# Performance work log

Hardware: AMD Instinct MI355X
Metric: run time of the kernel (lower is better)

Reference implementation:

```python
import jax, jax.numpy as jnp
import numpy as np

B, N, XD = 64, 512, 32  # batch, n_points, x_dims (feature columns); last 2 cols are t, y


def setup_inputs() -> dict:
    key = jax.random.key(0)
    xtys = jax.random.normal(key, (B, N, XD + 2), dtype=jnp.float32)
    return {"xtys": xtys}


def _linear_dml(xtys):
    b, n, D = xtys.shape
    d = D - 2
    xs = xtys[..., :d]          # (b, n, d) covariates
    ts = xtys[..., d]           # (b, n)   treatment
    ys = xtys[..., d + 1]       # (b, n)   outcome

    # Growing-prefix least squares via cumulative sufficient statistics.
    # For prefix i (rows 0..i): min-norm lstsq solution w = pinv(X^T X) X^T v == pinv(X) v,
    # matching torch.linalg.lstsq (gelsy/gelsd) semantics including rank-deficient prefixes.
    G = jnp.cumsum(jnp.einsum('bnd,bne->bnde', xs, xs), axis=1)      # (b,n,d,d) Gram
    Xty = jnp.cumsum(xs * ys[..., None], axis=1)                     # (b,n,d)
    Xtt = jnp.cumsum(xs * ts[..., None], axis=1)                     # (b,n,d)
    Sty = jnp.cumsum(ts * ys, axis=1)                                # (b,n)
    Stt = jnp.cumsum(ts * ts, axis=1)                                # (b,n)

    Ginv = jnp.linalg.pinv(G)                                        # batched pinv, (b,n,d,d)
    wy = jnp.einsum('bnde,bne->bnd', Ginv, Xty)
    wt = jnp.einsum('bnde,bne->bnd', Ginv, Xtt)

    # ate_i = <t_res, y_res> / <t_res, t_res> over prefix, expanded via the stats above.
    num = (Sty
           - jnp.einsum('bnd,bnd->bn', wt, Xty)
           - jnp.einsum('bnd,bnd->bn', wy, Xtt)
           + jnp.einsum('bnd,bnde,bne->bn', wt, G, wy))
    den = (Stt
           - 2.0 * jnp.einsum('bnd,bnd->bn', wt, Xtt)
           + jnp.einsum('bnd,bnde,bne->bn', wt, G, wt))
    safe = den > 0
    ate = jnp.where(safe, num / jnp.where(safe, den, 1.0), 0.0)      # min-norm: 0 when thats==0

    means = ate.at[:, 0].set(0.0)                                    # i==0 special case
    stds = jnp.zeros_like(means)                                     # module always appends zeros
    return means, 2.0 * jnp.log(stds)                                # -> -inf, as in the original


def reference(xtys):
    return _linear_dml(xtys)
```

## Files before the change

### kernel.cpp

```cpp
#include <hip/hip_runtime.h>
#include <math.h>
#include <utility>

#define BB 64
#define NN 512
#define DD 32
#define ZD 34
#define NE 595
#define WIN 8
#define NW 64
#define WACT 60

#define SEG 4
#define RS 128
#define KWS 16
#define CH 4
#define ECH 149
#define PSTRIDE 17

#define SPW 4

__device__ inline void ent2ij(int e, int& i, int& j) {
    int ii = 0, rem = e;
    while (rem >= ZD - ii) { rem -= (ZD - ii); ++ii; }
    i = ii; j = ii + rem;
}

template<int N> struct Pack { Pack<N - 1> head; float v; };
template<> struct Pack<1> { float v; };
template<int I, int N> __device__ __forceinline__ float& pget(Pack<N>& p) {
    static_assert(I < N, "oob");
    if constexpr (I == N - 1) return p.v;
    else return pget<I, N - 1>(p.head);
}

__device__ __forceinline__ float rdlane(float x, int srclane) {
    return __int_as_float(__builtin_amdgcn_readlane(__float_as_int(x), srclane));
}

__global__ __launch_bounds__(256) void dml_gram(const float* __restrict__ xtys,
                                                float* __restrict__ P,
                                                float* __restrict__ out) {
    const int t   = threadIdx.x;
    const int blk = blockIdx.x;
    const int c   = blk % CH;
    const int bg  = blk / CH;
    const int g   = bg % SEG;
    const int b   = bg / SEG;

    const int gid = blk * 256 + t;
    if (gid < BB * NN) out[BB * NN + gid] = 0.0f;
    if (gid < BB * DD) out[(gid >> 5) * NN + (gid & 31)] = 0.0f;

    __shared__ float zs[RS * ZD];
    const float* src = xtys + ((size_t)b * NN + (size_t)g * RS) * ZD;
    for (int u = t; u < RS * ZD; u += 256) zs[u] = src[u];
    __syncthreads();

    const int e = c * ECH + t;
    if (t < ECH && e < NE) {
        int i, j;
        ent2ij(e, i, j);
        float* pdst = P + (size_t)(b * SEG + g) * PSTRIDE * NE + e;
        double acc = 0.0;
#pragma unroll
        for (int k = 0; k < KWS; ++k) {
            pdst[k * NE] = (float)acc;
#pragma unroll
            for (int s8 = 0; s8 < WIN; ++s8) {
                const float* row = &zs[(k * WIN + s8) * ZD];
                acc = fma((double)row[i], (double)row[j], acc);
            }
        }
        pdst[KWS * NE] = (float)acc;
    }
}


template<int R> __device__ __forceinline__
float initval(int j, const float* snL, const float* zb) {
    if constexpr (R < DD) {
        float v = 0.0f;
        if (j < DD) {
            int i0 = (R < j) ? R : j;
            int j0 = (R < j) ? j : R;
            v = snL[i0 * ZD - (i0 * (i0 - 1)) / 2 + (j0 - i0)];
        } else if (j < DD + WIN) {
            v = zb[(j - DD) * ZD + R];
        } else if (j == 40) {
            v = snL[R * ZD - (R * (R - 1)) / 2 + (DD - R)];
        } else if (j == 41) {
            v = snL[R * ZD - (R * (R - 1)) / 2 + (DD + 1 - R)];
        }
        return v;
    } else if constexpr (R < DD + WIN) {
        return (j < DD) ? zb[(R - DD) * ZD + j] : 0.0f;
    } else if constexpr (R == 40) {
        return (j < DD) ? snL[j * ZD - (j * (j - 1)) / 2 + (DD - j)] : 0.0f;
    } else if constexpr (R == 41) {
        return (j < DD) ? snL[j * ZD - (j * (j - 1)) / 2 + (DD + 1 - j)] : 0.0f;
    } else {
        return 0.0f;
    }
}
template<int R> __device__ __forceinline__
void init_rec(Pack<48>& A, int j, const float* snL, const float* zb) {
    if constexpr (R < 48) {
        pget<R>(A) = initval<R>(j, snL, zb);
        init_rec<R + 1>(A, j, snL, zb);
    }
}

template<int K, int R> __device__ __forceinline__
void elim_rows(Pack<48>& A, float t) {
    if constexpr (R < DD + 10) {
        float fr = rdlane(pget<R>(A), K);
        pget<R>(A) = fmaf(-fr, t, pget<R>(A));
        elim_rows<K, R + 1>(A, t);
    }
}
template<int K> __device__ __forceinline__
void elim_step(Pack<48>& A) {
    float piv  = rdlane(pget<K>(A), K);
    float invp = (piv > 1e-30f) ? 1.0f / piv : 0.0f;
    float t    = invp * pget<K>(A);
    elim_rows<K, K + 1>(A, t);
}
template<int... Ks> __device__ __forceinline__
void elim_all(Pack<48>& A, std::integer_sequence<int, Ks...>) {
    ((elim_step<Ks>(A)), ...);
}

template<int R> __device__ __forceinline__
void kdump(Pack<48>& A, float* Kl, int c) {
    if constexpr (R < DD + 10) {
        Kl[(R - DD) * 10 + c] = -pget<R>(A);
        kdump<R + 1>(A, Kl, c);
    }
}

template<int L> __device__ __forceinline__
void tinit(Pack<96>& T, int m, const float* Kl, const float* zb) {
    if constexpr (L < 96) {
        constexpr int I = L / 12, J = L % 12;
        float v;
        if constexpr (J < 8) {
            float kij = (I < m && J < m) ? Kl[I * 10 + J] : 0.0f;
            v = kij + ((I == J) ? 1.0f : 0.0f);
        } else if constexpr (J == 8)  v = (I < m) ? Kl[I * 10 + 8] : 0.0f;
        else if constexpr (J == 9)    v = (I < m) ? zb[I * ZD + DD] : 0.0f;
        else if constexpr (J == 10)   v = (I < m) ? Kl[I * 10 + 9] : 0.0f;
        else                          v = (I < m) ? zb[I * ZD + DD + 1] : 0.0f;
        pget<L>(T) = v;
        tinit<L + 1>(T, m, Kl, zb);
    }
}
template<int K, int I, int J> __device__ __forceinline__
void gj_cols(Pack<96>& T, float f) {
    if constexpr (J < 12) {
        pget<I * 12 + J>(T) = fmaf(-f, pget<K * 12 + J>(T), pget<I * 12 + J>(T));
        gj_cols<K, I, J + 1>(T, f);
    }
}
template<int K, int I> __device__ __forceinline__
void gj_rows(Pack<96>& T, float invp) {
    if constexpr (I < 8) {
        if constexpr (I != K) {
            float f = pget<I * 12 + K>(T) * invp;
            gj_cols<K, I, K + 1>(T, f);
        }
        gj_rows<K, I + 1>(T, invp);
    }
}
template<int K> __device__ __forceinline__
void gj_step(Pack<96>& T) {
    float piv  = pget<K * 12 + K>(T);
    float invp = (piv > 1e-30f || piv < -1e-30f) ? 1.0f / piv : 0.0f;
    gj_rows<K, 0>(T, invp);
}
template<int... Ks> __device__ __forceinline__
void gj_all(Pack<96>& T, std::integer_sequence<int, Ks...>) {
    ((gj_step<Ks>(T)), ...);
}
template<int I> __device__ __forceinline__
void finacc(Pack<96>& T, int m, const float* Kl, const float* zb,
            double& dt, double& nt) {
    if constexpr (I < 8) {
        if (I < m) {
            float di   = pget<I * 12 + I>(T);
            float dinv = (di > 1e-30f || di < -1e-30f) ? 1.0f / di : 0.0f;
            double s1 = (double)(pget<I * 12 + 8>(T) * dinv);
            double s2 = (double)(pget<I * 12 + 9>(T) * dinv);
            double r1 = (double)(pget<I * 12 + 10>(T) * dinv);
            double r2 = (double)(pget<I * 12 + 11>(T) * dinv);
            double g  = (double)Kl[80 + I] - (double)zb[I * ZD + DD];
            dt += g * (s1 - s2);
            nt += g * (r1 - r2);
        }
        finacc<I + 1>(T, m, Kl, zb, dt, nt);
    }
}

__global__ __launch_bounds__(256) void dml_solve(const float* __restrict__ xtys,
                                                 const float* __restrict__ P,
                                                 float* __restrict__ out) {
    const int wid  = threadIdx.x >> 6;
    const int lane = threadIdx.x & 63;
    const int id   = blockIdx.x * SPW + wid;
    const int w    = (id % WACT) + 4;
    const int b    = id / WACT;
    const int g    = w >> 4;
    const int k    = w & 15;

    __shared__ float snL[SPW][NE];
    __shared__ float zb[SPW][WIN * ZD];
    __shared__ float Kl[SPW][100];
    float* snW = snL[wid];
    float* zbW = zb[wid];
    float* KlW = Kl[wid];

    const float* pb  = P + (size_t)b * SEG * PSTRIDE * NE;
    const float* src = xtys + ((size_t)b * NN + (size_t)w * WIN) * ZD;
    for (int u = lane; u < NE; u += 64) {
        float v = pb[(size_t)(g * PSTRIDE + k) * NE + u];
        for (int g2 = 0; g2 < g; ++g2)
            v += pb[(size_t)(g2 * PSTRIDE + KWS) * NE + u];
        snW[u] = v;
    }
    for (int u = lane; u < WIN * ZD; u += 64) zbW[u] = src[u];
    __syncthreads();

    Pack<48> A;
    init_rec<0>(A, lane, snW, zbW);

    elim_all(A, std::make_integer_sequence<int, DD>{});

    if (lane >= DD && lane < DD + 10) kdump<DD>(A, KlW, lane - DD);
    __syncthreads();

    if (lane < 8) {
        const int m = lane + 1;
        Pack<96> T;
        tinit<0>(T, m, KlW, zbW);
        gj_all(T, std::make_integer_sequence<int, 8>{});
        double dt = 0.0, nt = 0.0;
        finacc<0>(T, m, KlW, zbW, dt, nt);
        double Stt0 = (double)snW[592];
        double Sty0 = (double)snW[593];
        double den  = Stt0 - (double)KlW[88] + dt;
        double num  = Sty0 - (double)KlW[89] + nt;
        double val  = (den > 0.0) ? num / den : 0.0;
        if (!isfinite(val)) val = 0.0;
        out[b * NN + w * WIN + lane] = (float)val;
    }
}

extern "C" void kernel_launch(void* const* d_in, const int* in_sizes, int n_in,
                              void* d_out, int out_size, void* d_ws, size_t ws_size,
                              hipStream_t stream) {
    const float* xtys = (const float*)d_in[0];
    float* out = (float*)d_out;
    float* P = (float*)d_ws;

    hipLaunchKernelGGL(dml_gram, dim3(BB * SEG * CH), dim3(256), 0, stream, xtys, P, out);
    hipLaunchKernelGGL(dml_solve, dim3(BB * WACT / SPW), dim3(256), 0, stream, xtys, P, out);
}
```

Baseline: 108.7 us.

## Spread the small Gauss-Jordan solves across all wave lanes with bpermute

The final 8x12 Gauss-Jordan solve previously ran on only 8 lanes, each keeping a 96-float tableau in registers. It is now split so each of the 64 lanes owns one row of one of the 8 systems. Pivot rows are fetched with ds_bpermute and the per-system sums are reduced with width-8 xor shuffles. The change also precomputes the triangular-index offsets used when loading the Gram matrix. It drops the two block barriers and relies on each wave using only its own shared-memory slice, which cuts register pressure and serial tail work but depends on intra-wave LDS ordering for correctness.

After: 98.08 us. 1.11x faster.

```diff
diff --git a/kernel.cpp b/kernel.cpp
--- a/kernel.cpp
+++ b/kernel.cpp
@@ -36,6 +36,9 @@
 
 __device__ __forceinline__ float rdlane(float x, int srclane) {
     return __int_as_float(__builtin_amdgcn_readlane(__float_as_int(x), srclane));
+}
+__device__ __forceinline__ float bperm(int byteaddr, float x) {
+    return __int_as_float(__builtin_amdgcn_ds_bpermute(byteaddr, __float_as_int(x)));
 }
 
 __global__ __launch_bounds__(256) void dml_gram(const float* __restrict__ xtys,
@@ -78,36 +81,37 @@
 
 
 template<int R> __device__ __forceinline__
-float initval(int j, const float* snL, const float* zb) {
+float initval(int j, int off_j, int zoff, const float* snL, const float* zb) {
+    constexpr int RC = (R < DD) ? (R * ZD - (R * (R - 1)) / 2 - R) : 0;
     if constexpr (R < DD) {
         float v = 0.0f;
         if (j < DD) {
-            int i0 = (R < j) ? R : j;
-            int j0 = (R < j) ? j : R;
-            v = snL[i0 * ZD - (i0 * (i0 - 1)) / 2 + (j0 - i0)];
+            int idx = (R < j) ? (RC + j) : (off_j + R);
+            v = snL[idx];
         } else if (j < DD + WIN) {
-            v = zb[(j - DD) * ZD + R];
+            v = zb[zoff + R];
         } else if (j == 40) {
-            v = snL[R * ZD - (R * (R - 1)) / 2 + (DD - R)];
+            v = snL[RC + DD];
         } else if (j == 41) {
-            v = snL[R * ZD - (R * (R - 1)) / 2 + (DD + 1 - R)];
+            v = snL[RC + DD + 1];
         }
         return v;
     } else if constexpr (R < DD + WIN) {
         return (j < DD) ? zb[(R - DD) * ZD + j] : 0.0f;
     } else if constexpr (R == 40) {
-        return (j < DD) ? snL[j * ZD - (j * (j - 1)) / 2 + (DD - j)] : 0.0f;
+        return (j < DD) ? snL[off_j + DD] : 0.0f;
     } else if constexpr (R == 41) {
-        return (j < DD) ? snL[j * ZD - (j * (j - 1)) / 2 + (DD + 1 - j)] : 0.0f;
+        return (j < DD) ? snL[off_j + DD + 1] : 0.0f;
     } else {
         return 0.0f;
     }
 }
 template<int R> __device__ __forceinline__
-void init_rec(Pack<48>& A, int j, const float* snL, const float* zb) {
+void init_rec(Pack<48>& A, int j, int off_j, int zoff,
+              const float* snL, const float* zb) {
     if constexpr (R < 48) {
-        pget<R>(A) = initval<R>(j, snL, zb);
-        init_rec<R + 1>(A, j, snL, zb);
+        pget<R>(A) = initval<R>(j, off_j, zoff, snL, zb);
+        init_rec<R + 1>(A, j, off_j, zoff, snL, zb);
     }
 }
 
@@ -140,65 +144,40 @@
 }
 
 template<int L> __device__ __forceinline__
-void tinit(Pack<96>& T, int m, const float* Kl, const float* zb) {
-    if constexpr (L < 96) {
-        constexpr int I = L / 12, J = L % 12;
+void tinit(Pack<12>& T, int row, int sys, const float* Kl, const float* zb) {
+    if constexpr (L < 12) {
         float v;
-        if constexpr (J < 8) {
-            float kij = (I < m && J < m) ? Kl[I * 10 + J] : 0.0f;
-            v = kij + ((I == J) ? 1.0f : 0.0f);
-        } else if constexpr (J == 8)  v = (I < m) ? Kl[I * 10 + 8] : 0.0f;
-        else if constexpr (J == 9)    v = (I < m) ? zb[I * ZD + DD] : 0.0f;
-        else if constexpr (J == 10)   v = (I < m) ? Kl[I * 10 + 9] : 0.0f;
-        else                          v = (I < m) ? zb[I * ZD + DD + 1] : 0.0f;
+        if constexpr (L < 8) {
+            float kij = (row <= sys && L <= sys) ? Kl[row * 10 + L] : 0.0f;
+            v = kij + ((row == L) ? 1.0f : 0.0f);
+        } else if constexpr (L == 8)  v = (row <= sys) ? Kl[row * 10 + 8] : 0.0f;
+        else if constexpr (L == 9)    v = (row <= sys) ? zb[row * ZD + DD] : 0.0f;
+        else if constexpr (L == 10)   v = (row <= sys) ? Kl[row * 10 + 9] : 0.0f;
+        else                          v = (row <= sys) ? zb[row * ZD + DD + 1] : 0.0f;
         pget<L>(T) = v;
-        tinit<L + 1>(T, m, Kl, zb);
-    }
-}
-template<int K, int I, int J> __device__ __forceinline__
-void gj_cols(Pack<96>& T, float f) {
+        tinit<L + 1>(T, row, sys, Kl, zb);
+    }
+}
+template<int K, int J> __device__ __forceinline__
+void gjp_cols(Pack<12>& T, float f, int pb) {
     if constexpr (J < 12) {
-        pget<I * 12 + J>(T) = fmaf(-f, pget<K * 12 + J>(T), pget<I * 12 + J>(T));
-        gj_cols<K, I, J + 1>(T, f);
-    }
-}
-template<int K, int I> __device__ __forceinline__
-void gj_rows(Pack<96>& T, float invp) {
-    if constexpr (I < 8) {
-        if constexpr (I != K) {
-            float f = pget<I * 12 + K>(T) * invp;
-            gj_cols<K, I, K + 1>(T, f);
-        }
-        gj_rows<K, I + 1>(T, invp);
+        float pk = bperm(pb + 4 * K, pget<J>(T));
+        pget<J>(T) = fmaf(-f, pk, pget<J>(T));
+        gjp_cols<K, J + 1>(T, f, pb);
     }
 }
 template<int K> __device__ __forceinline__
-void gj_step(Pack<96>& T) {
-    float piv  = pget<K * 12 + K>(T);
-    float invp = (piv > 1e-30f || piv < -1e-30f) ? 1.0f / piv : 0.0f;
-    gj_rows<K, 0>(T, invp);
+void gjp_step(Pack<12>& T, int pb, int row, float& diag) {
+    float pkK  = bperm(pb + 4 * K, pget<K>(T));
+    float invp = (pkK > 1e-30f || pkK < -1e-30f) ? 1.0f / pkK : 0.0f;
+    float f    = (row == K) ? 0.0f : pget<K>(T) * invp;
+    gjp_cols<K, K + 1>(T, f, pb);
+    if (row == K) diag = pget<K>(T);
 }
 template<int... Ks> __device__ __forceinline__
-void gj_all(Pack<96>& T, std::integer_sequence<int, Ks...>) {
-    ((gj_step<Ks>(T)), ...);
-}
-template<int I> __device__ __forceinline__
-void finacc(Pack<96>& T, int m, const float* Kl, const float* zb,
-            double& dt, double& nt) {
-    if constexpr (I < 8) {
-        if (I < m) {
-            float di   = pget<I * 12 + I>(T);
-            float dinv = (di > 1e-30f || di < -1e-30f) ? 1.0f / di : 0.0f;
-            double s1 = (double)(pget<I * 12 + 8>(T) * dinv);
-            double s2 = (double)(pget<I * 12 + 9>(T) * dinv);
-            double r1 = (double)(pget<I * 12 + 10>(T) * dinv);
-            double r2 = (double)(pget<I * 12 + 11>(T) * dinv);
-            double g  = (double)Kl[80 + I] - (double)zb[I * ZD + DD];
-            dt += g * (s1 - s2);
-            nt += g * (r1 - r2);
-        }
-        finacc<I + 1>(T, m, Kl, zb, dt, nt);
-    }
+void gjp_all(Pack<12>& T, int pb, int row, float& diag,
+             std::integer_sequence<int, Ks...>) {
+    ((gjp_step<Ks>(T, pb, row, diag)), ...);
 }
 
 __global__ __launch_bounds__(256) void dml_solve(const float* __restrict__ xtys,
@@ -219,40 +198,57 @@
     float* zbW = zb[wid];
     float* KlW = Kl[wid];
 
-    const float* pb  = P + (size_t)b * SEG * PSTRIDE * NE;
-    const float* src = xtys + ((size_t)b * NN + (size_t)w * WIN) * ZD;
+    const float* pb_  = P + (size_t)b * SEG * PSTRIDE * NE;
+    const float* src  = xtys + ((size_t)b * NN + (size_t)w * WIN) * ZD;
     for (int u = lane; u < NE; u += 64) {
-        float v = pb[(size_t)(g * PSTRIDE + k) * NE + u];
+        float v = pb_[(size_t)(g * PSTRIDE + k) * NE + u];
         for (int g2 = 0; g2 < g; ++g2)
-            v += pb[(size_t)(g2 * PSTRIDE + KWS) * NE + u];
+            v += pb_[(size_t)(g2 * PSTRIDE + KWS) * NE + u];
         snW[u] = v;
     }
     for (int u = lane; u < WIN * ZD; u += 64) zbW[u] = src[u];
-    __syncthreads();
+
+    const int j     = lane;
+    const int off_j = j * (ZD - 1) - (j * (j - 1)) / 2;
+    const int zoff  = (j - DD) * ZD;
 
     Pack<48> A;
-    init_rec<0>(A, lane, snW, zbW);
+    init_rec<0>(A, j, off_j, zoff, snW, zbW);
 
     elim_all(A, std::make_integer_sequence<int, DD>{});
 
     if (lane >= DD && lane < DD + 10) kdump<DD>(A, KlW, lane - DD);
-    __syncthreads();
-
-    if (lane < 8) {
-        const int m = lane + 1;
-        Pack<96> T;
-        tinit<0>(T, m, KlW, zbW);
-        gj_all(T, std::make_integer_sequence<int, 8>{});
-        double dt = 0.0, nt = 0.0;
-        finacc<0>(T, m, KlW, zbW, dt, nt);
-        double Stt0 = (double)snW[592];
-        double Sty0 = (double)snW[593];
-        double den  = Stt0 - (double)KlW[88] + dt;
-        double num  = Sty0 - (double)KlW[89] + nt;
-        double val  = (den > 0.0) ? num / den : 0.0;
-        if (!isfinite(val)) val = 0.0;
-        out[b * NN + w * WIN + lane] = (float)val;
-    }
+
+    const int sys = lane >> 3;
+    const int row = lane & 7;
+    const int pb  = (threadIdx.x & ~7) << 2;
+
+    Pack<12> T;
+    tinit<0>(T, row, sys, KlW, zbW);
+    float diag = 1.0f;
+    gjp_all(T, pb, row, diag, std::make_integer_sequence<int, 8>{});
+
+    float dinv = (diag > 1e-30f || diag < -1e-30f) ? 1.0f / diag : 0.0f;
+    double s1 = (double)(pget<8>(T) * dinv);
+    double s2 = (double)(pget<9>(T) * dinv);
+    double r1 = (double)(pget<10>(T) * dinv);
+    double r2 = (double)(pget<11>(T) * dinv);
+    double gg = (double)KlW[80 + row] - (double)zbW[row * ZD + DD];
+    double cd = gg * (s1 - s2);
+    double cn = gg * (r1 - r2);
+#pragma unroll
+    for (int m = 1; m < 8; m <<= 1) {
+        cd += __shfl_xor(cd, m, 8);
+        cn += __shfl_xor(cn, m, 8);
+    }
+
+    double Stt0 = (double)snW[592];
+    double Sty0 = (double)snW[593];
+    double den  = Stt0 - (double)KlW[88] + cd;
+    double num  = Sty0 - (double)KlW[89] + cn;
+    double val  = (den > 0.0) ? num / den : 0.0;
+    if (!isfinite(val)) val = 0.0;
+    if (row == 0) out[b * NN + w * WIN + sys] = (float)val;
 }
 
 extern "C" void kernel_launch(void* const* d_in, const int* in_sizes, int n_in,
```
